# Performance work log

Measured on AMD Instinct MI355X. Metric: run time of the kernel, lower is better.

## Reference

```python
import jax, jax.numpy as jnp
import numpy as np

H = 8          # num_heads
NEG = -1e30    # masked-score value
EPS = 1e-5


def layer_norm(h, g, b):
    mu = jnp.mean(h, -1, keepdims=True)
    v = jnp.mean(jnp.square(h - mu), -1, keepdims=True)
    return (h - mu) * jax.lax.rsqrt(v + EPS) * g + b


def mha(q_in, kv_in, in_w, in_b, out_w, out_b, mask):
    # in_w: [3D, D] packed q/k/v projections (PyTorch MultiheadAttention layout)
    D = q_in.shape[-1]
    dh = D // H
    wq, wk, wv = in_w[:D], in_w[D:2 * D], in_w[2 * D:]
    bq, bk, bv = in_b[:D], in_b[D:2 * D], in_b[2 * D:]
    q = (q_in @ wq.T + bq).reshape(q_in.shape[0], q_in.shape[1], H, dh)
    k = (kv_in @ wk.T + bk).reshape(kv_in.shape[0], kv_in.shape[1], H, dh)
    v = (kv_in @ wv.T + bv).reshape(kv_in.shape[0], kv_in.shape[1], H, dh)
    s = jnp.einsum('bqhd,bkhd->bhqk', q, k) / jnp.sqrt(jnp.float32(dh))
    if mask is not None:
        s = s + mask  # [1,1,S,S] additive causal mask
    a = jax.nn.softmax(s, axis=-1)
    o = jnp.einsum('bhqk,bkhd->bqhd', a, v).reshape(q_in.shape[0], q_in.shape[1], D)
    return o @ out_w.T + out_b


def _forward(x, start_query, one_emb, zero_emb,
             sa_in_w, sa_in_b, sa_out_w, sa_out_b,
             ca_in_w, ca_in_b, ca_out_w, ca_out_b,
             lin1_w, lin1_b, lin2_w, lin2_b,
             ln_g, ln_b, cls_w, cls_b, label):
    B, S, D = x.shape
    n = label.shape[0]  # == S
    # Teacher-forced decoder inputs: [start_query, emb(label[0]), ..., emb(label[n-2])]
    tok = jnp.where((label[:-1] > 0.5)[:, None], one_emb[None, :], zero_emb[None, :])  # [n-1, D]
    tgt = jnp.concatenate([start_query[None, :], tok], axis=0)  # [n, D]
    h = jnp.broadcast_to(tgt[None], (B, n, D))
    causal = jnp.tril(jnp.ones((n, n), dtype=bool))
    mask = jnp.where(causal, 0.0, NEG).astype(x.dtype)[None, None]
    L = sa_in_w.shape[0]
    for l in range(L):
        # post-LN TransformerDecoderLayer (PyTorch default, relu FFN)
        sa = mha(h, h, sa_in_w[l], sa_in_b[l], sa_out_w[l], sa_out_b[l], mask)
        h = layer_norm(h + sa, ln_g[l, 0], ln_b[l, 0])
        ca = mha(h, x, ca_in_w[l], ca_in_b[l], ca_out_w[l], ca_out_b[l], None)
        h = layer_norm(h + ca, ln_g[l, 1], ln_b[l, 1])
        ff = jax.nn.relu(h @ lin1_w[l].T + lin1_b[l]) @ lin2_w[l].T + lin2_b[l]
        h = layer_norm(h + ff, ln_g[l, 2], ln_b[l, 2])
    # classifier + sigmoid; output[b, i] == decoder(tf[:1+i])[-1] of the original loop
    return jax.nn.sigmoid(h @ cls_w.T + cls_b)  # [B, n, 1]


def setup_inputs() -> dict:
    key = jax.random.key(0)
    ks = iter(jax.random.split(key, 32))
    B, S, D, FF, L = 8, 1024, 1024, 2048, 6

    def w(shape, s=0.02):
        return jax.random.normal(next(ks), shape, jnp.float32) * s

    return dict(
        x=jax.random.normal(next(ks), (B, S, D), jnp.float32),
        label=jax.random.uniform(next(ks), (S,), jnp.float32),
        start_query=jax.random.uniform(next(ks), (D,), jnp.float32),
        one_emb=jax.random.uniform(next(ks), (D,), jnp.float32),
        zero_emb=jax.random.uniform(next(ks), (D,), jnp.float32),
        sa_in_w=w((L, 3 * D, D)), sa_in_b=jnp.zeros((L, 3 * D), jnp.float32),
        sa_out_w=w((L, D, D)), sa_out_b=jnp.zeros((L, D), jnp.float32),
        ca_in_w=w((L, 3 * D, D)), ca_in_b=jnp.zeros((L, 3 * D), jnp.float32),
        ca_out_w=w((L, D, D)), ca_out_b=jnp.zeros((L, D), jnp.float32),
        lin1_w=w((L, FF, D)), lin1_b=jnp.zeros((L, FF), jnp.float32),
        lin2_w=w((L, D, FF)), lin2_b=jnp.zeros((L, D), jnp.float32),
        ln_g=jnp.ones((L, 3, D), jnp.float32), ln_b=jnp.zeros((L, 3, D), jnp.float32),
        cls_w=w((1, D)), cls_b=jnp.zeros((1,), jnp.float32),
    )


def reference(x, label, start_query, one_emb, zero_emb,
              sa_in_w, sa_in_b, sa_out_w, sa_out_b,
              ca_in_w, ca_in_b, ca_out_w, ca_out_b,
              lin1_w, lin1_b, lin2_w, lin2_b,
              ln_g, ln_b, cls_w, cls_b):
    return _forward(x, start_query, one_emb, zero_emb,
                    sa_in_w, sa_in_b, sa_out_w, sa_out_b,
                    ca_in_w, ca_in_b, ca_out_w, ca_out_b,
                    lin1_w, lin1_b, lin2_w, lin2_b,
                    ln_g, ln_b, cls_w, cls_b, label)
```

## Files before the change

kernel.cpp:

```cpp
#include <hip/hip_runtime.h>
#include <stdint.h>

typedef __attribute__((ext_vector_type(8))) short short8;
typedef __attribute__((ext_vector_type(4))) float f32x4;
typedef __attribute__((ext_vector_type(4))) float float4v;
typedef __attribute__((ext_vector_type(4))) unsigned short ushort4v;

__device__ __forceinline__ float b2f(short u) {
  union { float f; uint32_t i; } v; v.i = ((uint32_t)(unsigned short)u) << 16; return v.f;
}
__device__ __forceinline__ short f2b(float f) {
  uint32_t x = __float_as_uint(f);
  uint32_t r = (x + 0x7fffu + ((x >> 16) & 1u)) >> 16;
  return (short)r;
}
__device__ __forceinline__ void gload16(const short* g, short* l) {
  __builtin_amdgcn_global_load_lds((__attribute__((address_space(1))) const void*)g,
                                   (__attribute__((address_space(3))) void*)l, 16, 0, 0);
}

__global__ void f2b_kernel(const float* __restrict__ in, short* __restrict__ out, int n4) {
  int i = blockIdx.x * blockDim.x + threadIdx.x;
  int stride = gridDim.x * blockDim.x;
  for (; i < n4; i += stride) {
    float4v v = *((const float4v*)in + i);
    ushort4v o;
    o[0] = (unsigned short)f2b(v[0]); o[1] = (unsigned short)f2b(v[1]);
    o[2] = (unsigned short)f2b(v[2]); o[3] = (unsigned short)f2b(v[3]);
    *((ushort4v*)out + i) = o;
  }
}

__global__ void h0_kernel(const float* __restrict__ label, const float* __restrict__ sq,
                          const float* __restrict__ onee, const float* __restrict__ zeroe,
                          short* __restrict__ h) {
  int i = blockIdx.x;
  const float* src = (i == 0) ? sq : (label[i - 1] > 0.5f ? onee : zeroe);
  int d = threadIdx.x * 4;
  float4v v = *(const float4v*)(src + d);
  ushort4v o;
  o[0] = (unsigned short)f2b(v[0]); o[1] = (unsigned short)f2b(v[1]);
  o[2] = (unsigned short)f2b(v[2]); o[3] = (unsigned short)f2b(v[3]);
#pragma unroll
  for (int b = 0; b < 8; ++b)
    *(ushort4v*)(h + ((size_t)b * 1024 + i) * 1024 + d) = o;
}

template <int EPI>
__global__ __launch_bounds__(256) void gemm_bt(const short* __restrict__ A,
                                               const short* __restrict__ W,
                                               const float* __restrict__ bias,
                                               short* __restrict__ C,
                                               int M, int N, int K) {
  __shared__ short a_lds[128 * 64];
  __shared__ short b_lds[128 * 64];
  const int tid = threadIdx.x, lane = tid & 63, w = tid >> 6;
  const int g = lane >> 4, l15 = lane & 15;
  const int nbx = N >> 7;
  int nwg = gridDim.x;
  int orig = blockIdx.x;
  int cpx = nwg >> 3;
  int id = (orig & 7) * cpx + (orig >> 3);
  int bx = id % nbx, by = id / nbx;
  const size_t rowA = (size_t)by * 128, colB = (size_t)bx * 128;
  const int wm = w >> 1, wn = w & 1;

  f32x4 acc[4][4];
#pragma unroll
  for (int i = 0; i < 4; ++i)
#pragma unroll
    for (int j = 0; j < 4; ++j) acc[i][j] = (f32x4){0.f, 0.f, 0.f, 0.f};

  for (int kt = 0; kt < K; kt += 64) {
#pragma unroll
    for (int c = 0; c < 4; ++c) {
      int ch = w * 4 + c;
      int r = ch * 8 + (lane >> 3);
      int u = lane & 7, us = u ^ (r & 7);
      gload16(A + (rowA + r) * K + kt + us * 8, (short*)a_lds + ch * 512);
      gload16(W + (colB + r) * K + kt + us * 8, (short*)b_lds + ch * 512);
    }
    __syncthreads();
#pragma unroll
    for (int t = 0; t < 2; ++t) {
      short8 af[4], bf[4];
#pragma unroll
      for (int i = 0; i < 4; ++i) {
        int ra = wm * 64 + i * 16 + l15;
        int ua = (4 * t + g) ^ (ra & 7);
        af[i] = *(const short8*)((const char*)a_lds + ra * 128 + ua * 16);
        int rb = wn * 64 + i * 16 + l15;
        int ub = (4 * t + g) ^ (rb & 7);
        bf[i] = *(const short8*)((const char*)b_lds + rb * 128 + ub * 16);
      }
#pragma unroll
      for (int i = 0; i < 4; ++i)
#pragma unroll
        for (int j = 0; j < 4; ++j)
          acc[i][j] = __builtin_amdgcn_mfma_f32_16x16x32_bf16(af[i], bf[j], acc[i][j], 0, 0, 0);
    }
    __syncthreads();
  }
  float bv[4];
#pragma unroll
  for (int j = 0; j < 4; ++j) bv[j] = bias[colB + wn * 64 + j * 16 + l15];
#pragma unroll
  for (int i = 0; i < 4; ++i) {
    size_t row = rowA + wm * 64 + i * 16 + g * 4;
#pragma unroll
    for (int j = 0; j < 4; ++j) {
      size_t col = colB + wn * 64 + j * 16 + l15;
#pragma unroll
      for (int r = 0; r < 4; ++r) {
        float v = acc[i][j][r] + bv[j];
        if (EPI == 1) v = fmaxf(v, 0.f);
        C[(row + r) * N + col] = f2b(v);
      }
    }
  }
}

__global__ __launch_bounds__(256) void tv_kernel(const short* __restrict__ src, int ld, int voff,
                                                 short* __restrict__ vt) {
  __shared__ short t[64 * 72];
  const int kt = blockIdx.x * 64, dt = blockIdx.y * 64, bh = blockIdx.z;
  const int b = bh >> 3, hh = bh & 7;
  const short* s = src + (size_t)(b * 1024 + kt) * ld + voff + hh * 128 + dt;
#pragma unroll
  for (int p = 0; p < 2; ++p) {
    int idx = p * 256 + threadIdx.x;
    int r = idx >> 3, u = idx & 7;
    *(short8*)&t[r * 72 + u * 8] = *(const short8*)&s[(size_t)r * ld + u * 8];
  }
  __syncthreads();
#pragma unroll
  for (int p = 0; p < 2; ++p) {
    int idx = p * 256 + threadIdx.x;
    int dd = idx >> 3, u = idx & 7;
    short8 o;
#pragma unroll
    for (int j = 0; j < 8; ++j) o[j] = t[(u * 8 + j) * 72 + dd];
    *(short8*)&vt[((size_t)bh * 128 + dt + dd) * 1024 + kt + u * 8] = o;
  }
}

template <bool CAUSAL>
__global__ __launch_bounds__(256, 2) void attn_kernel(const short* __restrict__ Qb, int ldq, int qoff,
                                                      const short* __restrict__ Kb, int ldk, int koff,
                                                      const short* __restrict__ Vt,
                                                      short* __restrict__ Ob) {
  __shared__ short k_lds[64 * 128];
  __shared__ short v_lds[128 * 64];
  __shared__ short p_lds[4 * 32 * 72];
  const int tid = threadIdx.x, lane = tid & 63, w = tid >> 6;
  const int g = lane >> 4, l15 = lane & 15;
  const int bh = blockIdx.y, b = bh >> 3, hh = bh & 7;
  const int q0 = blockIdx.x * 128;
  const float scale = 0.08838834764831845f;

  short8 qf[2][4];
#pragma unroll
  for (int fm = 0; fm < 2; ++fm) {
    int row = q0 + w * 32 + fm * 16 + l15;
    const short* qp = Qb + (size_t)(b * 1024 + row) * ldq + qoff + hh * 128;
#pragma unroll
    for (int t = 0; t < 4; ++t) qf[fm][t] = *(const short8*)(qp + t * 32 + g * 8);
  }

  f32x4 oacc[2][8];
  float m_st[2][4], l_st[2][4];
#pragma unroll
  for (int fm = 0; fm < 2; ++fm) {
#pragma unroll
    for (int fo = 0; fo < 8; ++fo) oacc[fm][fo] = (f32x4){0.f, 0.f, 0.f, 0.f};
#pragma unroll
    for (int r = 0; r < 4; ++r) { m_st[fm][r] = -3.0e38f; l_st[fm][r] = 0.f; }
  }

  const int ktend = CAUSAL ? (q0 >> 6) + 1 : 15;
  for (int kt = 0; kt <= ktend; ++kt) {
    __syncthreads();
#pragma unroll
    for (int c = 0; c < 4; ++c) {
      int ch = w * 4 + c;
      int r = ch * 4 + (lane >> 4);
      int u = lane & 15, us = u ^ (r & 7);
      gload16(Kb + (size_t)(b * 1024 + kt * 64 + r) * ldk + koff + hh * 128 + us * 8,
              (short*)k_lds + ch * 512);
    }
#pragma unroll
    for (int c = 0; c < 4; ++c) {
      int ch = w * 4 + c;
      int d = ch * 8 + (lane >> 3);
      int u = lane & 7, us = u ^ (d & 7);
      gload16(Vt + ((size_t)bh * 128 + d) * 1024 + kt * 64 + us * 8, (short*)v_lds + ch * 512);
    }
    __syncthreads();

    f32x4 sacc[2][4];
#pragma unroll
    for (int fm = 0; fm < 2; ++fm)
#pragma unroll
      for (int fn = 0; fn < 4; ++fn) sacc[fm][fn] = (f32x4){0.f, 0.f, 0.f, 0.f};
#pragma unroll
    for (int t = 0; t < 4; ++t) {
      short8 kf[4];
#pragma unroll
      for (int fn = 0; fn < 4; ++fn) {
        int rowk = fn * 16 + l15;
        int u = (4 * t + g) ^ (rowk & 7);
        kf[fn] = *(const short8*)((const char*)k_lds + rowk * 256 + u * 16);
      }
#pragma unroll
      for (int fm = 0; fm < 2; ++fm)
#pragma unroll
        for (int fn = 0; fn < 4; ++fn)
          sacc[fm][fn] = __builtin_amdgcn_mfma_f32_16x16x32_bf16(qf[fm][t], kf[fn], sacc[fm][fn], 0, 0, 0);
    }

#pragma unroll
    for (int fm = 0; fm < 2; ++fm)
#pragma unroll
      for (int reg = 0; reg < 4; ++reg) {
        float sv[4];
        float mt = -3.0e38f;
#pragma unroll
        for (int fn = 0; fn < 4; ++fn) {
          float s = sacc[fm][fn][reg] * scale;
          if (CAUSAL) {
            int kg = kt * 64 + fn * 16 + l15;
            int qg = q0 + w * 32 + fm * 16 + g * 4 + reg;
            if (kg > qg) s = -1e30f;
          }
          sv[fn] = s;
          mt = fmaxf(mt, s);
        }
#pragma unroll
        for (int off = 1; off < 16; off <<= 1) mt = fmaxf(mt, __shfl_xor(mt, off));
        float mo = m_st[fm][reg];
        float mn = fmaxf(mo, mt);
        float corr = __expf(mo - mn);
        float ps = 0.f;
#pragma unroll
        for (int fn = 0; fn < 4; ++fn) {
          float p = __expf(sv[fn] - mn);
          ps += p;
          p_lds[w * 2304 + (fm * 16 + g * 4 + reg) * 72 + fn * 16 + l15] = f2b(p);
        }
#pragma unroll
        for (int off = 1; off < 16; off <<= 1) ps += __shfl_xor(ps, off);
        l_st[fm][reg] = l_st[fm][reg] * corr + ps;
        m_st[fm][reg] = mn;
#pragma unroll
        for (int fo = 0; fo < 8; ++fo) oacc[fm][fo][reg] *= corr;
      }
    __syncthreads();

#pragma unroll
    for (int t = 0; t < 2; ++t) {
      short8 pf[2];
#pragma unroll
      for (int fm = 0; fm < 2; ++fm)
        pf[fm] = *(const short8*)(p_lds + w * 2304 + (fm * 16 + l15) * 72 + t * 32 + g * 8);
#pragma unroll
      for (int fo = 0; fo < 8; ++fo) {
        int rowd = fo * 16 + l15;
        int u = (4 * t + g) ^ (rowd & 7);
        short8 vf = *(const short8*)((const char*)v_lds + rowd * 128 + u * 16);
#pragma unroll
        for (int fm = 0; fm < 2; ++fm)
          oacc[fm][fo] = __builtin_amdgcn_mfma_f32_16x16x32_bf16(pf[fm], vf, oacc[fm][fo], 0, 0, 0);
      }
    }
  }

#pragma unroll
  for (int fm = 0; fm < 2; ++fm)
#pragma unroll
    for (int fo = 0; fo < 8; ++fo)
#pragma unroll
      for (int reg = 0; reg < 4; ++reg) {
        int row = q0 + w * 32 + fm * 16 + g * 4 + reg;
        int col = hh * 128 + fo * 16 + l15;
        float o = oacc[fm][fo][reg] / l_st[fm][reg];
        Ob[(size_t)(b * 1024 + row) * 1024 + col] = f2b(o);
      }
}

__global__ __launch_bounds__(128) void ln_kernel(const short* __restrict__ h,
                                                 const short* __restrict__ delta,
                                                 const float* __restrict__ gg,
                                                 const float* __restrict__ bb,
                                                 short* __restrict__ out) {
  __shared__ float red[4];
  const int row = blockIdx.x, tid = threadIdx.x;
  const short8 hv = *(const short8*)(h + (size_t)row * 1024 + tid * 8);
  const short8 dv = *(const short8*)(delta + (size_t)row * 1024 + tid * 8);
  float x[8];
  float s = 0.f, s2 = 0.f;
#pragma unroll
  for (int j = 0; j < 8; ++j) {
    x[j] = b2f(hv[j]) + b2f(dv[j]);
    s += x[j];
    s2 += x[j] * x[j];
  }
#pragma unroll
  for (int o = 1; o < 64; o <<= 1) { s += __shfl_xor(s, o); s2 += __shfl_xor(s2, o); }
  if ((tid & 63) == 0) { red[(tid >> 6) * 2] = s; red[(tid >> 6) * 2 + 1] = s2; }
  __syncthreads();
  s = red[0] + red[2];
  s2 = red[1] + red[3];
  const float mu = s * (1.f / 1024.f);
  const float var = s2 * (1.f / 1024.f) - mu * mu;
  const float rs = rsqrtf(var + 1e-5f);
  short8 o;
#pragma unroll
  for (int j = 0; j < 8; ++j) {
    int d = tid * 8 + j;
    o[j] = f2b((x[j] - mu) * rs * gg[d] + bb[d]);
  }
  *(short8*)(out + (size_t)row * 1024 + tid * 8) = o;
}

__global__ __launch_bounds__(256) void cls_kernel(const short* __restrict__ h,
                                                  const float* __restrict__ wv,
                                                  const float* __restrict__ bias,
                                                  float* __restrict__ out) {
  const int lane = threadIdx.x & 63, w = threadIdx.x >> 6;
  const int row = blockIdx.x * 4 + w;
  const short* hp = h + (size_t)row * 1024 + lane * 16;
  float sum = 0.f;
#pragma unroll
  for (int i = 0; i < 2; ++i) {
    short8 v = *(const short8*)(hp + i * 8);
#pragma unroll
    for (int j = 0; j < 8; ++j) sum += b2f(v[j]) * wv[lane * 16 + i * 8 + j];
  }
#pragma unroll
  for (int o = 1; o < 64; o <<= 1) sum += __shfl_xor(sum, o);
  if (lane == 0) {
    float z = sum + bias[0];
    out[row] = 1.f / (1.f + __expf(-z));
  }
}

#define O_SA_IN  ((size_t)0)
#define O_SA_OUT ((size_t)18874368)
#define O_CA_IN  ((size_t)25165824)
#define O_CA_OUT ((size_t)44040192)
#define O_LIN1   ((size_t)50331648)
#define O_LIN2   ((size_t)62914560)
#define O_X      ((size_t)75497472)
#define O_H      ((size_t)83886080)
#define O_QKV    ((size_t)92274688)
#define O_ATTN   ((size_t)117440512)
#define O_DELTA  ((size_t)125829120)
#define O_VT     ((size_t)134217728)
#define O_FF1    ((size_t)142606336)

extern "C" void kernel_launch(void* const* d_in, const int* in_sizes, int n_in,
                              void* d_out, int out_size, void* d_ws, size_t ws_size,
                              hipStream_t stream) {
  const float* x = (const float*)d_in[0];
  const float* label = (const float*)d_in[1];
  const float* sq = (const float*)d_in[2];
  const float* onee = (const float*)d_in[3];
  const float* zeroe = (const float*)d_in[4];
  const float* sa_in_w = (const float*)d_in[5];
  const float* sa_in_b = (const float*)d_in[6];
  const float* sa_out_w = (const float*)d_in[7];
  const float* sa_out_b = (const float*)d_in[8];
  const float* ca_in_w = (const float*)d_in[9];
  const float* ca_in_b = (const float*)d_in[10];
  const float* ca_out_w = (const float*)d_in[11];
  const float* ca_out_b = (const float*)d_in[12];
  const float* lin1_w = (const float*)d_in[13];
  const float* lin1_b = (const float*)d_in[14];
  const float* lin2_w = (const float*)d_in[15];
  const float* lin2_b = (const float*)d_in[16];
  const float* ln_g = (const float*)d_in[17];
  const float* ln_b = (const float*)d_in[18];
  const float* cls_w = (const float*)d_in[19];
  const float* cls_b = (const float*)d_in[20];

  short* ws = (short*)d_ws;
  short* w_sa_in = ws + O_SA_IN;
  short* w_sa_out = ws + O_SA_OUT;
  short* w_ca_in = ws + O_CA_IN;
  short* w_ca_out = ws + O_CA_OUT;
  short* w_lin1 = ws + O_LIN1;
  short* w_lin2 = ws + O_LIN2;
  short* xb = ws + O_X;
  short* hbuf = ws + O_H;
  short* qkv = ws + O_QKV;
  short* kvb = qkv + 8388608;
  short* attnb = ws + O_ATTN;
  short* delta = ws + O_DELTA;
  short* vt = ws + O_VT;
  short* ff1 = ws + O_FF1;

  f2b_kernel<<<4096, 256, 0, stream>>>(sa_in_w, w_sa_in, 18874368 / 4);
  f2b_kernel<<<4096, 256, 0, stream>>>(sa_out_w, w_sa_out, 6291456 / 4);
  f2b_kernel<<<4096, 256, 0, stream>>>(ca_in_w, w_ca_in, 18874368 / 4);
  f2b_kernel<<<4096, 256, 0, stream>>>(ca_out_w, w_ca_out, 6291456 / 4);
  f2b_kernel<<<4096, 256, 0, stream>>>(lin1_w, w_lin1, 12582912 / 4);
  f2b_kernel<<<4096, 256, 0, stream>>>(lin2_w, w_lin2, 12582912 / 4);
  f2b_kernel<<<4096, 256, 0, stream>>>(x, xb, 8388608 / 4);
  h0_kernel<<<1024, 256, 0, stream>>>(label, sq, onee, zeroe, hbuf);

  for (int l = 0; l < 6; ++l) {
    gemm_bt<0><<<1536, 256, 0, stream>>>(hbuf, w_sa_in + (size_t)l * 3145728,
                                         sa_in_b + (size_t)l * 3072, qkv, 8192, 3072, 1024);
    tv_kernel<<<dim3(16, 2, 64), 256, 0, stream>>>(qkv, 3072, 2048, vt);
    attn_kernel<true><<<dim3(8, 64), 256, 0, stream>>>(qkv, 3072, 0, qkv, 3072, 1024, vt, attnb);
    gemm_bt<0><<<512, 256, 0, stream>>>(attnb, w_sa_out + (size_t)l * 1048576,
                                        sa_out_b + (size_t)l * 1024, delta, 8192, 1024, 1024);
    ln_kernel<<<8192, 128, 0, stream>>>(hbuf, delta, ln_g + (size_t)(l * 3 + 0) * 1024,
                                        ln_b + (size_t)(l * 3 + 0) * 1024, hbuf);
    gemm_bt<0><<<512, 256, 0, stream>>>(hbuf, w_ca_in + (size_t)l * 3145728,
                                        ca_in_b + (size_t)l * 3072, qkv, 8192, 1024, 1024);
    gemm_bt<0><<<1024, 256, 0, stream>>>(xb, w_ca_in + (size_t)l * 3145728 + 1048576,
                                         ca_in_b + (size_t)l * 3072 + 1024, kvb, 8192, 2048, 1024);
    tv_kernel<<<dim3(16, 2, 64), 256, 0, stream>>>(kvb, 2048, 1024, vt);
    attn_kernel<false><<<dim3(8, 64), 256, 0, stream>>>(qkv, 1024, 0, kvb, 2048, 0, vt, attnb);
    gemm_bt<0><<<512, 256, 0, stream>>>(attnb, w_ca_out + (size_t)l * 1048576,
                                        ca_out_b + (size_t)l * 1024, delta, 8192, 1024, 1024);
    ln_kernel<<<8192, 128, 0, stream>>>(hbuf, delta, ln_g + (size_t)(l * 3 + 1) * 1024,
                                        ln_b + (size_t)(l * 3 + 1) * 1024, hbuf);
    gemm_bt<1><<<1024, 256, 0, stream>>>(hbuf, w_lin1 + (size_t)l * 2097152,
                                         lin1_b + (size_t)l * 2048, ff1, 8192, 2048, 1024);
    gemm_bt<0><<<512, 256, 0, stream>>>(ff1, w_lin2 + (size_t)l * 2097152,
                                        lin2_b + (size_t)l * 1024, delta, 8192, 1024, 2048);
    ln_kernel<<<8192, 128, 0, stream>>>(hbuf, delta, ln_g + (size_t)(l * 3 + 2) * 1024,
                                        ln_b + (size_t)(l * 3 + 2) * 1024, hbuf);
  }
  cls_kernel<<<2048, 256, 0, stream>>>(hbuf, cls_w, cls_b, (float*)d_out);
}
```

Baseline: 3.140 ms.

## Switch GEMMs to 256x256 double-buffered tiles and reorder causal attention blocks

Replaces the 128x128 single-buffered GEMM with a 512-thread 256x256 tile kernel. It prefetches the next K-slice into a second LDS buffer while computing on the current one, and splits the MFMA work into barrier-separated phases that raise wave priority around the matrix ops. The larger tile raises operand reuse per LDS load and hides global-load latency, at the cost of 128 KB of LDS, higher register pressure, and fewer workgroups on the smaller N=1024 GEMMs (128 blocks). Causal attention query blocks are remapped so heavy and light tiles are interleaved across the grid for better load balance.

```diff
diff --git a/kernel.cpp b/kernel.cpp
--- a/kernel.cpp
+++ b/kernel.cpp
@@ -46,67 +46,138 @@
     *(ushort4v*)(h + ((size_t)b * 1024 + i) * 1024 + d) = o;
 }
 
+__device__ __forceinline__ void stage256(const short* __restrict__ mat, size_t rc0,
+                                         int K, int kt, short* dst, int w, int lane) {
+  const int us = (lane & 7) ^ (lane >> 3);
+  const int rlo = lane >> 3;
+#pragma unroll
+  for (int q = 0; q < 8; ++q) {
+    int c = (w & 3) * 8 + q;
+    int half = c >> 4, ci = c & 15;
+    int rih = ci * 8 + rlo;
+    gload16(mat + (rc0 + half * 128 + rih) * (size_t)K + kt * 64 + us * 8,
+            dst + ((w >> 2) * 32 + c) * 512);
+  }
+}
+
 template <int EPI>
-__global__ __launch_bounds__(256) void gemm_bt(const short* __restrict__ A,
-                                               const short* __restrict__ W,
-                                               const float* __restrict__ bias,
-                                               short* __restrict__ C,
-                                               int M, int N, int K) {
-  __shared__ short a_lds[128 * 64];
-  __shared__ short b_lds[128 * 64];
+__global__ __launch_bounds__(512, 2) void gemm256(const short* __restrict__ A,
+                                                  const short* __restrict__ W,
+                                                  const float* __restrict__ bias,
+                                                  short* __restrict__ C,
+                                                  int M, int N, int K) {
+  __shared__ short lds[2 * 4 * 8192];
   const int tid = threadIdx.x, lane = tid & 63, w = tid >> 6;
   const int g = lane >> 4, l15 = lane & 15;
-  const int nbx = N >> 7;
-  int nwg = gridDim.x;
-  int orig = blockIdx.x;
-  int cpx = nwg >> 3;
+  const int wm = w >> 2, wn = w & 3;
+  const int nbx = N >> 8;
+  int nwg = gridDim.x, orig = blockIdx.x, cpx = nwg >> 3;
   int id = (orig & 7) * cpx + (orig >> 3);
   int bx = id % nbx, by = id / nbx;
-  const size_t rowA = (size_t)by * 128, colB = (size_t)bx * 128;
-  const int wm = w >> 1, wn = w & 1;
-
-  f32x4 acc[4][4];
-#pragma unroll
-  for (int i = 0; i < 4; ++i)
+  const size_t rowA = (size_t)by * 256, colB = (size_t)bx * 256;
+  const int NT = K >> 6;
+
+  const short* smat = (w < 4) ? A : W;
+  const size_t src0 = (w < 4) ? rowA : colB;
+
+  f32x4 acc[8][4];
+#pragma unroll
+  for (int i = 0; i < 8; ++i)
 #pragma unroll
     for (int j = 0; j < 4; ++j) acc[i][j] = (f32x4){0.f, 0.f, 0.f, 0.f};
 
-  for (int kt = 0; kt < K; kt += 64) {
-#pragma unroll
-    for (int c = 0; c < 4; ++c) {
-      int ch = w * 4 + c;
-      int r = ch * 8 + (lane >> 3);
-      int u = lane & 7, us = u ^ (r & 7);
-      gload16(A + (rowA + r) * K + kt + us * 8, (short*)a_lds + ch * 512);
-      gload16(W + (colB + r) * K + kt + us * 8, (short*)b_lds + ch * 512);
-    }
-    __syncthreads();
-#pragma unroll
-    for (int t = 0; t < 2; ++t) {
-      short8 af[4], bf[4];
-#pragma unroll
-      for (int i = 0; i < 4; ++i) {
-        int ra = wm * 64 + i * 16 + l15;
-        int ua = (4 * t + g) ^ (ra & 7);
-        af[i] = *(const short8*)((const char*)a_lds + ra * 128 + ua * 16);
-        int rb = wn * 64 + i * 16 + l15;
-        int ub = (4 * t + g) ^ (rb & 7);
-        bf[i] = *(const short8*)((const char*)b_lds + rb * 128 + ub * 16);
-      }
-#pragma unroll
-      for (int i = 0; i < 4; ++i)
-#pragma unroll
-        for (int j = 0; j < 4; ++j)
-          acc[i][j] = __builtin_amdgcn_mfma_f32_16x16x32_bf16(af[i], bf[j], acc[i][j], 0, 0, 0);
-    }
-    __syncthreads();
-  }
+  int sxz0 = g ^ (l15 & 7);
+  int sxz1 = (4 + g) ^ (l15 & 7);
+  const short* abase = lds + wm * 8192 + l15 * 64;
+  const short* bbase = lds + (2 + (wn >> 1)) * 8192 + ((wn & 1) * 64 + l15) * 64;
+
+  stage256(smat, src0, K, 0, lds, w, lane);
+  asm volatile("s_waitcnt vmcnt(0)" ::: "memory");
+  __builtin_amdgcn_s_barrier();
+
+  int p = 0;
+  for (int t = 0; t < NT; ++t) {
+    if (t + 1 < NT) stage256(smat, src0, K, t + 1, lds + (p ^ 1) * 32768, w, lane);
+    const int po = p * 32768;
+    short8 af[4][2], bf0[2][2], bf1[2][2];
+
+#pragma unroll
+    for (int i = 0; i < 4; ++i) {
+      af[i][0] = *(const short8*)(abase + po + i * 1024 + sxz0 * 8);
+      af[i][1] = *(const short8*)(abase + po + i * 1024 + sxz1 * 8);
+    }
+#pragma unroll
+    for (int j = 0; j < 2; ++j) {
+      bf0[j][0] = *(const short8*)(bbase + po + j * 1024 + sxz0 * 8);
+      bf0[j][1] = *(const short8*)(bbase + po + j * 1024 + sxz1 * 8);
+    }
+    __builtin_amdgcn_s_barrier();
+    __builtin_amdgcn_s_setprio(1);
+#pragma unroll
+    for (int i = 0; i < 4; ++i)
+#pragma unroll
+      for (int j = 0; j < 2; ++j)
+#pragma unroll
+        for (int ks = 0; ks < 2; ++ks)
+          acc[i][j] = __builtin_amdgcn_mfma_f32_16x16x32_bf16(af[i][ks], bf0[j][ks], acc[i][j], 0, 0, 0);
+    __builtin_amdgcn_s_setprio(0);
+    __builtin_amdgcn_s_barrier();
+
+#pragma unroll
+    for (int j = 0; j < 2; ++j) {
+      bf1[j][0] = *(const short8*)(bbase + po + (2 + j) * 1024 + sxz0 * 8);
+      bf1[j][1] = *(const short8*)(bbase + po + (2 + j) * 1024 + sxz1 * 8);
+    }
+    __builtin_amdgcn_s_barrier();
+    __builtin_amdgcn_s_setprio(1);
+#pragma unroll
+    for (int i = 0; i < 4; ++i)
+#pragma unroll
+      for (int j = 0; j < 2; ++j)
+#pragma unroll
+        for (int ks = 0; ks < 2; ++ks)
+          acc[i][2 + j] = __builtin_amdgcn_mfma_f32_16x16x32_bf16(af[i][ks], bf1[j][ks], acc[i][2 + j], 0, 0, 0);
+    __builtin_amdgcn_s_setprio(0);
+    __builtin_amdgcn_s_barrier();
+
+#pragma unroll
+    for (int i = 0; i < 4; ++i) {
+      af[i][0] = *(const short8*)(abase + po + (64 + i * 16) * 64 + sxz0 * 8);
+      af[i][1] = *(const short8*)(abase + po + (64 + i * 16) * 64 + sxz1 * 8);
+    }
+    __builtin_amdgcn_s_barrier();
+    __builtin_amdgcn_s_setprio(1);
+#pragma unroll
+    for (int i = 0; i < 4; ++i)
+#pragma unroll
+      for (int j = 0; j < 2; ++j)
+#pragma unroll
+        for (int ks = 0; ks < 2; ++ks)
+          acc[4 + i][2 + j] = __builtin_amdgcn_mfma_f32_16x16x32_bf16(af[i][ks], bf1[j][ks], acc[4 + i][2 + j], 0, 0, 0);
+    __builtin_amdgcn_s_setprio(0);
+    __builtin_amdgcn_s_barrier();
+
+    __builtin_amdgcn_s_setprio(1);
+#pragma unroll
+    for (int i = 0; i < 4; ++i)
+#pragma unroll
+      for (int j = 0; j < 2; ++j)
+#pragma unroll
+        for (int ks = 0; ks < 2; ++ks)
+          acc[4 + i][j] = __builtin_amdgcn_mfma_f32_16x16x32_bf16(af[i][ks], bf0[j][ks], acc[4 + i][j], 0, 0, 0);
+    __builtin_amdgcn_s_setprio(0);
+
+    asm volatile("s_waitcnt vmcnt(0)" ::: "memory");
+    __builtin_amdgcn_s_barrier();
+    p ^= 1;
+  }
+
   float bv[4];
 #pragma unroll
   for (int j = 0; j < 4; ++j) bv[j] = bias[colB + wn * 64 + j * 16 + l15];
 #pragma unroll
-  for (int i = 0; i < 4; ++i) {
-    size_t row = rowA + wm * 64 + i * 16 + g * 4;
+  for (int i = 0; i < 8; ++i) {
+    size_t row = rowA + wm * 128 + i * 16 + g * 4;
 #pragma unroll
     for (int j = 0; j < 4; ++j) {
       size_t col = colB + wn * 64 + j * 16 + l15;
@@ -155,7 +226,9 @@
   const int tid = threadIdx.x, lane = tid & 63, w = tid >> 6;
   const int g = lane >> 4, l15 = lane & 15;
   const int bh = blockIdx.y, b = bh >> 3, hh = bh & 7;
-  const int q0 = blockIdx.x * 128;
+  int qi = blockIdx.x;
+  if (CAUSAL) qi = (qi < 4) ? qi : 11 - qi;
+  const int q0 = qi * 128;
   const float scale = 0.08838834764831845f;
 
   short8 qf[2][4];
@@ -409,27 +482,27 @@
   h0_kernel<<<1024, 256, 0, stream>>>(label, sq, onee, zeroe, hbuf);
 
   for (int l = 0; l < 6; ++l) {
-    gemm_bt<0><<<1536, 256, 0, stream>>>(hbuf, w_sa_in + (size_t)l * 3145728,
-                                         sa_in_b + (size_t)l * 3072, qkv, 8192, 3072, 1024);
+    gemm256<0><<<384, 512, 0, stream>>>(hbuf, w_sa_in + (size_t)l * 3145728,
+                                        sa_in_b + (size_t)l * 3072, qkv, 8192, 3072, 1024);
     tv_kernel<<<dim3(16, 2, 64), 256, 0, stream>>>(qkv, 3072, 2048, vt);
     attn_kernel<true><<<dim3(8, 64), 256, 0, stream>>>(qkv, 3072, 0, qkv, 3072, 1024, vt, attnb);
-    gemm_bt<0><<<512, 256, 0, stream>>>(attnb, w_sa_out + (size_t)l * 1048576,
+    gemm256<0><<<128, 512, 0, stream>>>(attnb, w_sa_out + (size_t)l * 1048576,
                                         sa_out_b + (size_t)l * 1024, delta, 8192, 1024, 1024);
     ln_kernel<<<8192, 128, 0, stream>>>(hbuf, delta, ln_g + (size_t)(l * 3 + 0) * 1024,
                                         ln_b + (size_t)(l * 3 + 0) * 1024, hbuf);
-    gemm_bt<0><<<512, 256, 0, stream>>>(hbuf, w_ca_in + (size_t)l * 3145728,
+    gemm256<0><<<128, 512, 0, stream>>>(hbuf, w_ca_in + (size_t)l * 3145728,
                                         ca_in_b + (size_t)l * 3072, qkv, 8192, 1024, 1024);
-    gemm_bt<0><<<1024, 256, 0, stream>>>(xb, w_ca_in + (size_t)l * 3145728 + 1048576,
-                                         ca_in_b + (size_t)l * 3072 + 1024, kvb, 8192, 2048, 1024);
+    gemm256<0><<<256, 512, 0, stream>>>(xb, w_ca_in + (size_t)l * 3145728 + 1048576,
+                                        ca_in_b + (size_t)l * 3072 + 1024, kvb, 8192, 2048, 1024);
     tv_kernel<<<dim3(16, 2, 64), 256, 0, stream>>>(kvb, 2048, 1024, vt);
     attn_kernel<false><<<dim3(8, 64), 256, 0, stream>>>(qkv, 1024, 0, kvb, 2048, 0, vt, attnb);
-    gemm_bt<0><<<512, 256, 0, stream>>>(attnb, w_ca_out + (size_t)l * 1048576,
+    gemm256<0><<<128, 512, 0, stream>>>(attnb, w_ca_out + (size_t)l * 1048576,
                                         ca_out_b + (size_t)l * 1024, delta, 8192, 1024, 1024);
     ln_kernel<<<8192, 128, 0, stream>>>(hbuf, delta, ln_g + (size_t)(l * 3 + 1) * 1024,
                                         ln_b + (size_t)(l * 3 + 1) * 1024, hbuf);
-    gemm_bt<1><<<1024, 256, 0, stream>>>(hbuf, w_lin1 + (size_t)l * 2097152,
-                                         lin1_b + (size_t)l * 2048, ff1, 8192, 2048, 1024);
-    gemm_bt<0><<<512, 256, 0, stream>>>(ff1, w_lin2 + (size_t)l * 2097152,
+    gemm256<1><<<256, 512, 0, stream>>>(hbuf, w_lin1 + (size_t)l * 2097152,
+                                        lin1_b + (size_t)l * 2048, ff1, 8192, 2048, 1024);
+    gemm256<0><<<128, 512, 0, stream>>>(ff1, w_lin2 + (size_t)l * 2097152,
                                         lin2_b + (size_t)l * 1024, delta, 8192, 1024, 2048);
     ln_kernel<<<8192, 128, 0, stream>>>(hbuf, delta, ln_g + (size_t)(l * 3 + 2) * 1024,
                                         ln_b + (size_t)(l * 3 + 2) * 1024, hbuf);
```

After: 3.259 ms. +3.8%, slower.
